# Kernel optimization log

Hardware: AMD Instinct MI355X
Metric: run time of the kernel (lower is better)

Reference implementation:

```python
import jax, jax.numpy as jnp
import numpy as np
import math

B, T, C = 4, 2048, 1024
NH = 16
HD = C // NH


def setup_inputs() -> dict:
    key = jax.random.key(0)
    ks = jax.random.split(key, 10)
    s = 0.02
    x = jax.random.normal(ks[0], (B, T, C), dtype=jnp.float32)
    W_qkv = jax.random.normal(ks[1], (C, 3 * C), dtype=jnp.float32) * s
    b_qkv = jnp.zeros((3 * C,), dtype=jnp.float32)
    W_proj = jax.random.normal(ks[2], (C, C), dtype=jnp.float32) * s
    b_proj = jnp.zeros((C,), dtype=jnp.float32)
    asym_mean, asym_std = 1.0, 0.7
    q_scale = jax.random.normal(ks[3], (NH, HD), dtype=jnp.float32) * asym_std + asym_mean
    q_bias = jax.random.normal(ks[4], (NH, HD), dtype=jnp.float32) * asym_std + asym_mean
    k_scale = jax.random.normal(ks[5], (NH, HD), dtype=jnp.float32) * asym_std + asym_mean
    k_bias = jax.random.normal(ks[6], (NH, HD), dtype=jnp.float32) * asym_std + asym_mean
    return {"x": x, "W_qkv": W_qkv, "b_qkv": b_qkv, "W_proj": W_proj,
            "b_proj": b_proj, "q_scale": q_scale, "q_bias": q_bias,
            "k_scale": k_scale, "k_bias": k_bias}


def reference(x, W_qkv, b_qkv, W_proj, b_proj, q_scale, q_bias, k_scale, k_bias):
    Bx, Tx, Cx = x.shape
    qkv = x @ W_qkv + b_qkv                       # [B,T,3C]
    q, k, v = jnp.split(qkv, 3, axis=-1)
    # [B,T,C] -> [B,NH,T,HD]
    reshape = lambda t: t.reshape(Bx, Tx, NH, HD).transpose(0, 2, 1, 3)
    q, k, v = reshape(q), reshape(k), reshape(v)
    # per-head affine scaling of Q/K
    q = q * q_scale[None, :, None, :] + q_bias[None, :, None, :]
    k = k * k_scale[None, :, None, :] + k_bias[None, :, None, :]
    scores = jnp.einsum('bhqd,bhkd->bhqk', q, k) / math.sqrt(HD)  # [B,NH,T,T]
    causal = jnp.tril(jnp.ones((Tx, Tx), dtype=bool))
    scores = jnp.where(causal[None, None], scores, -jnp.inf)
    att = jax.nn.softmax(scores, axis=-1)
    y = jnp.einsum('bhqk,bhkd->bhqd', att, v)     # [B,NH,T,HD]
    y = y.transpose(0, 2, 1, 3).reshape(Bx, Tx, Cx)
    return y @ W_proj + b_proj
```

## Files before the change

kernel.cpp:

```cpp
#include <hip/hip_runtime.h>
#include <hip/hip_bf16.h>

typedef unsigned short u16;
typedef __attribute__((ext_vector_type(8))) short short8;
typedef __attribute__((ext_vector_type(4))) float floatx4;

#define B_SZ 4
#define T_SZ 2048
#define C_SZ 1024
#define NH_SZ 16
#define HD_SZ 64
#define M_TOT 8192
#define K_DIM 1024

#define QSCALE 0.1803368801111204f

#define OFF_XB   ((size_t)16)
#define OFF_WQT  (OFF_XB + 8388608)
#define OFF_WPT  (OFF_WQT + 3145728)
#define OFF_PB   (OFF_WPT + 1048576)
#define OFF_Q    (OFF_PB + 8192)
#define OFF_K    (OFF_Q + 8388608)
#define OFF_V    (OFF_K + 8388608)
#define OFF_Y    (OFF_V + 8388608)
#define PB_BQKV  0
#define PB_BPROJ 3072
#define PB_QSC   4096
#define PB_QBI   5120
#define PB_KSC   6144
#define PB_KBI   7168

__device__ __forceinline__ float bf2f(u16 u) {
    return __uint_as_float(((unsigned)u) << 16);
}
__device__ __forceinline__ u16 f2bf(float f) {
    unsigned x = __float_as_uint(f);
    unsigned r = (x + 0x7fffu + ((x >> 16) & 1u)) >> 16;
    return (u16)r;
}
__device__ __forceinline__ u16 f2bf_fast(float f) {
    return (u16)((__float_as_uint(f) + 0x8000u) >> 16);
}
__device__ __forceinline__ void gl_lds16(const u16* g, u16* l) {
    __builtin_amdgcn_global_load_lds(
        (const __attribute__((address_space(1))) void*)g,
        (__attribute__((address_space(3))) void*)l, 16, 0, 0);
}

__global__ __launch_bounds__(256) void detect_k(const u16* __restrict__ x,
                                                int* __restrict__ flag) {
    __shared__ int cnt;
    if (threadIdx.x == 0) cnt = 0;
    __syncthreads();
    int bad = 0;
    for (int i = threadIdx.x; i < 512; i += 256) {
        float v = fabsf(bf2f(x[i]));
        if (v > 1024.0f || (v != 0.0f && v < 9.5367431640625e-7f)) bad++;
    }
    atomicAdd(&cnt, bad);
    __syncthreads();
    if (threadIdx.x == 0) flag[0] = (cnt > 16) ? 1 : 0;
}

__global__ __launch_bounds__(256) void prep_k(
        const void* __restrict__ x,
        const void* __restrict__ Wqkv, const void* __restrict__ Wproj,
        const void* __restrict__ bqkv, const void* __restrict__ bproj,
        const void* __restrict__ qsc, const void* __restrict__ qbi,
        const void* __restrict__ ksc, const void* __restrict__ kbi,
        u16* __restrict__ xb, u16* __restrict__ Wt_qkv,
        u16* __restrict__ Wt_proj, u16* __restrict__ pb,
        const int* __restrict__ flag) {
    __shared__ u16 t[32][33];
    const int blk = blockIdx.x;
    const int isf = flag[0];
    if (blk < 8192) {
        const int i = blk * 256 + threadIdx.x;
        if (isf) {
            const float4 v = ((const float4*)x)[i];
            ushort4 o;
            o.x = f2bf(v.x); o.y = f2bf(v.y); o.z = f2bf(v.z); o.w = f2bf(v.w);
            ((ushort4*)xb)[i] = o;
        } else {
            ((ushort4*)xb)[i] = ((const ushort4*)x)[i];
        }
        return;
    }
    if (blk < 8200) {
        const int i4 = (blk - 8192) * 256 + threadIdx.x;
        if (i4 >= 2048) return;
        const int e = i4 * 4;
        const void* src; int off;
        if (e < 3072)      { src = bqkv;  off = e; }
        else if (e < 4096) { src = bproj; off = e - 3072; }
        else if (e < 5120) { src = qsc;   off = e - 4096; }
        else if (e < 6144) { src = qbi;   off = e - 5120; }
        else if (e < 7168) { src = ksc;   off = e - 6144; }
        else               { src = kbi;   off = e - 7168; }
        ushort4 o;
        if (isf) {
            const float4 v = *(const float4*)((const float*)src + off);
            o.x = f2bf(v.x); o.y = f2bf(v.y); o.z = f2bf(v.z); o.w = f2bf(v.w);
        } else {
            o = *(const ushort4*)((const u16*)src + off);
        }
        *(ushort4*)&pb[e] = o;
        return;
    }
    const void* in; u16* out; int R, C, idx;
    if (blk < 11272) { idx = blk - 8200;  in = Wqkv;  out = Wt_qkv;  R = 1024; C = 3072; }
    else             { idx = blk - 11272; in = Wproj; out = Wt_proj; R = 1024; C = 1024; }
    const int nbx = C >> 5;
    const int c0 = (idx % nbx) * 32, r0 = (idx / nbx) * 32;
    const int tx = threadIdx.x & 31, ty = threadIdx.x >> 5;
    for (int i = 0; i < 4; i++) {
        int r = ty + i * 8;
        size_t gi = (size_t)(r0 + r) * C + c0 + tx;
        t[r][tx] = isf ? f2bf(((const float*)in)[gi]) : ((const u16*)in)[gi];
    }
    __syncthreads();
    for (int i = 0; i < 4; i++) {
        int cr = ty + i * 8;
        out[(size_t)(c0 + cr) * R + r0 + tx] = t[tx][cr];
    }
}

__global__ __launch_bounds__(256) void qkv_gemm(
        const u16* __restrict__ X, const u16* __restrict__ Wt,
        const u16* __restrict__ pb,
        u16* __restrict__ Qb, u16* __restrict__ Kb, u16* __restrict__ Vb) {
    __shared__ __align__(16) u16 As[128 * 64];
    __shared__ __align__(16) u16 Bs[128 * 64];
    const int bm = blockIdx.y * 128, bn = blockIdx.x * 128;
    const int tid = threadIdx.x;
    const int lane = tid & 63, wave = tid >> 6;
    const int quad = lane >> 4, l16 = lane & 15;
    const int wm = (wave & 1) * 64, wn = (wave >> 1) * 64;
    const int lrow = lane >> 3;
    const int lcol = ((lane & 7) ^ lrow) * 8;

    floatx4 acc[4][4];
    for (int mi = 0; mi < 4; mi++)
        for (int ni = 0; ni < 4; ni++) acc[mi][ni] = 0.f;

    for (int k0 = 0; k0 < K_DIM; k0 += 64) {
        __syncthreads();
        for (int j = 0; j < 4; j++) {
            const int rb = wave * 32 + j * 8;
            gl_lds16(&X[(size_t)(bm + rb + lrow) * K_DIM + k0 + lcol], &As[rb * 64]);
            gl_lds16(&Wt[(size_t)(bn + rb + lrow) * K_DIM + k0 + lcol], &Bs[rb * 64]);
        }
        __syncthreads();
        for (int kk = 0; kk < 64; kk += 32) {
            const int cb = kk >> 3;
            const int slot = ((cb + quad) ^ (l16 & 7)) * 8;
            short8 a[4], b[4];
            for (int mi = 0; mi < 4; mi++)
                a[mi] = *(const short8*)&As[(wm + mi * 16 + l16) * 64 + slot];
            for (int ni = 0; ni < 4; ni++)
                b[ni] = *(const short8*)&Bs[(wn + ni * 16 + l16) * 64 + slot];
            for (int mi = 0; mi < 4; mi++)
                for (int ni = 0; ni < 4; ni++)
                    acc[mi][ni] = __builtin_amdgcn_mfma_f32_16x16x32_bf16(
                        a[mi], b[ni], acc[mi][ni], 0, 0, 0);
        }
    }

    const int sec = bn >> 10;
    const int bb = bm >> 11;
    const int tbase = bm & 2047;
    for (int mi = 0; mi < 4; mi++) {
        for (int ni = 0; ni < 4; ni++) {
            const int col = bn + wn + ni * 16 + l16;
            const int cmod = col & 1023;
            const int h = cmod >> 6, d = cmod & 63;
            const float bv = bf2f(pb[PB_BQKV + col]);
            if (sec == 2) {
                const int t0 = tbase + wm + mi * 16 + quad * 4;
                ushort4 pk;
                pk.x = f2bf(acc[mi][ni][0] + bv);
                pk.y = f2bf(acc[mi][ni][1] + bv);
                pk.z = f2bf(acc[mi][ni][2] + bv);
                pk.w = f2bf(acc[mi][ni][3] + bv);
                *(ushort4*)&Vb[(((size_t)(bb * NH_SZ + h)) * HD_SZ + d) * T_SZ + t0] = pk;
            } else {
                float sA, sB;
                if (sec == 0) {
                    sA = bf2f(pb[PB_QSC + h * 64 + d]) * QSCALE;
                    sB = bf2f(pb[PB_QBI + h * 64 + d]) * QSCALE;
                } else {
                    sA = bf2f(pb[PB_KSC + h * 64 + d]);
                    sB = bf2f(pb[PB_KBI + h * 64 + d]);
                }
                u16* dstbuf = (sec == 0) ? Qb : Kb;
                for (int r = 0; r < 4; r++) {
                    const int t = tbase + wm + mi * 16 + quad * 4 + r;
                    float v = (acc[mi][ni][r] + bv) * sA + sB;
                    dstbuf[(((size_t)(bb * NH_SZ + h)) * T_SZ + t) * HD_SZ + d] = f2bf(v);
                }
            }
        }
    }
}

__global__ __launch_bounds__(512) void attn_k(const u16* __restrict__ Qb,
                                              const u16* __restrict__ Kb,
                                              const u16* __restrict__ Vtg,
                                              u16* __restrict__ Y) {
    __shared__ __align__(16) u16 Ks[64 * 64];
    __shared__ __align__(16) u16 Vs[64 * 64];
    __shared__ __align__(16) u16 Ps[8 * 16 * 88];
    const int blk = blockIdx.x;
    const int head = blk & 63;
    const int p = blk >> 6;
    const int b = head >> 4, h = head & 15;
    const int tid = threadIdx.x, lane = tid & 63, w = tid >> 6;
    const int quad = lane >> 4, l16 = lane & 15;
    const size_t qk_off = (size_t)head * (T_SZ * HD_SZ);
    const size_t v_off = (size_t)head * (HD_SZ * T_SZ);
    u16* psw = &Ps[w * 1408];
    const int lr = lane >> 3;
    const int lc = ((lane & 7) ^ lr) * 8;
    const int sl0 = ((quad) ^ (l16 & 7)) * 8;
    const int sl1 = ((4 + quad) ^ (l16 & 7)) * 8;

    short8 ones;
    for (int j = 0; j < 8; j++) ones[j] = (short)0x3F80;

    for (int tile = 0; tile < 2; tile++) {
        const int qt = tile ? p : (15 - p);
        const int q0 = qt * 128;
        const int rbase = q0 + w * 16;
        const int q = rbase + l16;

        const short8 aq0 = *(const short8*)&Qb[qk_off + (size_t)q * HD_SZ + quad * 8];
        const short8 aq1 = *(const short8*)&Qb[qk_off + (size_t)q * HD_SZ + 32 + quad * 8];

        floatx4 o[4];
        for (int mi = 0; mi < 4; mi++) o[mi] = 0.f;
        float m_run = -1e30f, l_run = 0.f;

        for (int k0 = 0; k0 < q0 + 128; k0 += 64) {
            __syncthreads();
            gl_lds16(&Kb[qk_off + (size_t)(k0 + w * 8 + lr) * HD_SZ + lc], &Ks[w * 512]);
            gl_lds16(&Vtg[v_off + (size_t)(w * 8 + lr) * T_SZ + k0 + lc], &Vs[w * 512]);
            __syncthreads();
            if (k0 > rbase + 15) continue;

            floatx4 s[4];
            for (int ni = 0; ni < 4; ni++) s[ni] = 0.f;
            for (int ni = 0; ni < 4; ni++)
                s[ni] = __builtin_amdgcn_mfma_f32_16x16x32_bf16(
                    *(const short8*)&Ks[(ni * 16 + l16) * 64 + sl0], aq0, s[ni], 0, 0, 0);
            for (int ni = 0; ni < 4; ni++)
                s[ni] = __builtin_amdgcn_mfma_f32_16x16x32_bf16(
                    *(const short8*)&Ks[(ni * 16 + l16) * 64 + sl1], aq1, s[ni], 0, 0, 0);

            if (k0 + 63 > rbase) {
                for (int ni = 0; ni < 4; ni++)
                    for (int r = 0; r < 4; r++) {
                        int key = k0 + ni * 16 + quad * 4 + r;
                        if (key > q) s[ni][r] = -1e30f;
                    }
            }

            float mx = fmaxf(fmaxf(s[0][0], s[0][1]), fmaxf(s[0][2], s[0][3]));
            for (int ni = 1; ni < 4; ni++)
                mx = fmaxf(mx, fmaxf(fmaxf(s[ni][0], s[ni][1]),
                                     fmaxf(s[ni][2], s[ni][3])));
            mx = fmaxf(mx, __shfl_xor(mx, 16, 64));
            mx = fmaxf(mx, __shfl_xor(mx, 32, 64));
            const float mnew = fmaxf(m_run, mx);
            const float alpha = exp2f(m_run - mnew);
            for (int ni = 0; ni < 4; ni++)
                for (int r = 0; r < 4; r++)
                    s[ni][r] = exp2f(s[ni][r] - mnew);
            m_run = mnew;
            for (int mi = 0; mi < 4; mi++) o[mi] *= alpha;

            for (int ni = 0; ni < 4; ni++) {
                ushort4 pk;
                pk.x = f2bf_fast(s[ni][0]); pk.y = f2bf_fast(s[ni][1]);
                pk.z = f2bf_fast(s[ni][2]); pk.w = f2bf_fast(s[ni][3]);
                *(ushort4*)&psw[l16 * 88 + ni * 16 + quad * 4] = pk;
            }

            floatx4 s4 = 0.f;
            for (int kk = 0; kk < 64; kk += 32) {
                short8 pfr = *(const short8*)&psw[l16 * 88 + kk + quad * 8];
                const int vsl = (kk == 0) ? sl0 : sl1;
                s4 = __builtin_amdgcn_mfma_f32_16x16x32_bf16(ones, pfr, s4, 0, 0, 0);
                for (int mi = 0; mi < 4; mi++) {
                    short8 vfr = *(const short8*)&Vs[(mi * 16 + l16) * 64 + vsl];
                    o[mi] = __builtin_amdgcn_mfma_f32_16x16x32_bf16(vfr, pfr, o[mi], 0, 0, 0);
                }
            }
            l_run = l_run * alpha + s4[0];
        }

        const float inv = 1.0f / l_run;
        u16* yrow = &Y[(((size_t)b * T_SZ + q) * NH_SZ + h) * HD_SZ];
        for (int mi = 0; mi < 4; mi++) {
            ushort4 pk;
            pk.x = f2bf_fast(o[mi][0] * inv); pk.y = f2bf_fast(o[mi][1] * inv);
            pk.z = f2bf_fast(o[mi][2] * inv); pk.w = f2bf_fast(o[mi][3] * inv);
            *(ushort4*)&yrow[mi * 16 + quad * 4] = pk;
        }
    }
}

__global__ __launch_bounds__(256) void proj_gemm(const u16* __restrict__ Yin,
                                                 const u16* __restrict__ Wt,
                                                 const u16* __restrict__ pb,
                                                 void* __restrict__ out,
                                                 const int* __restrict__ flag) {
    __shared__ __align__(16) u16 As[128 * 64];
    __shared__ __align__(16) u16 Bs[128 * 64];
    const int isf = flag[0];
    const int bm = blockIdx.y * 128, bn = blockIdx.x * 128;
    const int tid = threadIdx.x;
    const int lane = tid & 63, wave = tid >> 6;
    const int quad = lane >> 4, l16 = lane & 15;
    const int wm = (wave & 1) * 64, wn = (wave >> 1) * 64;
    const int lrow = lane >> 3;
    const int lcol = ((lane & 7) ^ lrow) * 8;

    floatx4 acc[4][4];
    for (int mi = 0; mi < 4; mi++)
        for (int ni = 0; ni < 4; ni++) acc[mi][ni] = 0.f;

    for (int k0 = 0; k0 < K_DIM; k0 += 64) {
        __syncthreads();
        for (int j = 0; j < 4; j++) {
            const int rb = wave * 32 + j * 8;
            gl_lds16(&Yin[(size_t)(bm + rb + lrow) * K_DIM + k0 + lcol], &As[rb * 64]);
            gl_lds16(&Wt[(size_t)(bn + rb + lrow) * K_DIM + k0 + lcol], &Bs[rb * 64]);
        }
        __syncthreads();
        for (int kk = 0; kk < 64; kk += 32) {
            const int cb = kk >> 3;
            const int slot = ((cb + quad) ^ (l16 & 7)) * 8;
            short8 a[4], b[4];
            for (int mi = 0; mi < 4; mi++)
                a[mi] = *(const short8*)&As[(wm + mi * 16 + l16) * 64 + slot];
            for (int ni = 0; ni < 4; ni++)
                b[ni] = *(const short8*)&Bs[(wn + ni * 16 + l16) * 64 + slot];
            for (int mi = 0; mi < 4; mi++)
                for (int ni = 0; ni < 4; ni++)
                    acc[mi][ni] = __builtin_amdgcn_mfma_f32_16x16x32_bf16(
                        a[mi], b[ni], acc[mi][ni], 0, 0, 0);
        }
    }

    for (int mi = 0; mi < 4; mi++) {
        for (int ni = 0; ni < 4; ni++) {
            const int col = bn + wn + ni * 16 + l16;
            const float bv = bf2f(pb[PB_BPROJ + col]);
            for (int r = 0; r < 4; r++) {
                const int row = bm + wm + mi * 16 + quad * 4 + r;
                const float v = acc[mi][ni][r] + bv;
                if (isf) ((float*)out)[(size_t)row * C_SZ + col] = v;
                else     ((u16*)out)[(size_t)row * C_SZ + col] = f2bf(v);
            }
        }
    }
}

extern "C" void kernel_launch(void* const* d_in, const int* in_sizes, int n_in,
                              void* d_out, int out_size, void* d_ws, size_t ws_size,
                              hipStream_t stream) {
    const void* x     = d_in[0];
    const void* Wqkv  = d_in[1];
    const void* bqkv  = d_in[2];
    const void* Wproj = d_in[3];
    const void* bproj = d_in[4];
    const void* qsc   = d_in[5];
    const void* qbi   = d_in[6];
    const void* ksc   = d_in[7];
    const void* kbi   = d_in[8];

    u16* ws = (u16*)d_ws;
    int* flag    = (int*)d_ws;
    u16* xb      = ws + OFF_XB;
    u16* Wt_qkv  = ws + OFF_WQT;
    u16* Wt_proj = ws + OFF_WPT;
    u16* pb      = ws + OFF_PB;
    u16* Qb      = ws + OFF_Q;
    u16* Kb      = ws + OFF_K;
    u16* Vb      = ws + OFF_V;
    u16* Yb      = ws + OFF_Y;

    detect_k<<<1, 256, 0, stream>>>((const u16*)x, flag);
    prep_k<<<12296, 256, 0, stream>>>(x, Wqkv, Wproj, bqkv, bproj,
                                      qsc, qbi, ksc, kbi,
                                      xb, Wt_qkv, Wt_proj, pb, flag);
    qkv_gemm<<<dim3(24, 64), 256, 0, stream>>>(xb, Wt_qkv, pb, Qb, Kb, Vb);
    attn_k<<<dim3(512), 512, 0, stream>>>(Qb, Kb, Vb, Yb);
    proj_gemm<<<dim3(8, 64), 256, 0, stream>>>(Yb, Wt_proj, pb, d_out, flag);
}
```

Measured before the change: 307.9 us.

## Double attention key tile to 128 with causal-aware active-key trimming; fold detect into prep

```diff
diff --git a/kernel.cpp b/kernel.cpp
--- a/kernel.cpp
+++ b/kernel.cpp
@@ -46,20 +46,13 @@
         (const __attribute__((address_space(1))) void*)g,
         (__attribute__((address_space(3))) void*)l, 16, 0, 0);
 }
-
-__global__ __launch_bounds__(256) void detect_k(const u16* __restrict__ x,
-                                                int* __restrict__ flag) {
-    __shared__ int cnt;
-    if (threadIdx.x == 0) cnt = 0;
-    __syncthreads();
-    int bad = 0;
-    for (int i = threadIdx.x; i < 512; i += 256) {
-        float v = fabsf(bf2f(x[i]));
-        if (v > 1024.0f || (v != 0.0f && v < 9.5367431640625e-7f)) bad++;
-    }
-    atomicAdd(&cnt, bad);
-    __syncthreads();
-    if (threadIdx.x == 0) flag[0] = (cnt > 16) ? 1 : 0;
+__device__ __forceinline__ int detect_isf(const u16* xx, int lane) {
+    float v0 = fabsf(bf2f(xx[lane * 2]));
+    float v1 = fabsf(bf2f(xx[lane * 2 + 1]));
+    int b0 = (v0 > 1024.0f) || (v0 != 0.0f && v0 < 9.5367431640625e-7f);
+    int b1 = (v1 > 1024.0f) || (v1 != 0.0f && v1 < 9.5367431640625e-7f);
+    unsigned long long ba = __ballot(b0), bb = __ballot(b1);
+    return (__popcll(ba) + __popcll(bb)) > 8;
 }
 
 __global__ __launch_bounds__(256) void prep_k(
@@ -70,10 +63,11 @@
         const void* __restrict__ ksc, const void* __restrict__ kbi,
         u16* __restrict__ xb, u16* __restrict__ Wt_qkv,
         u16* __restrict__ Wt_proj, u16* __restrict__ pb,
-        const int* __restrict__ flag) {
+        int* __restrict__ flag) {
     __shared__ u16 t[32][33];
     const int blk = blockIdx.x;
-    const int isf = flag[0];
+    const int isf = detect_isf((const u16*)x, threadIdx.x & 63);
+    if (blk == 0 && threadIdx.x == 0) flag[0] = isf;
     if (blk < 8192) {
         const int i = blk * 256 + threadIdx.x;
         if (isf) {
@@ -207,9 +201,9 @@
                                               const u16* __restrict__ Kb,
                                               const u16* __restrict__ Vtg,
                                               u16* __restrict__ Y) {
-    __shared__ __align__(16) u16 Ks[64 * 64];
-    __shared__ __align__(16) u16 Vs[64 * 64];
-    __shared__ __align__(16) u16 Ps[8 * 16 * 88];
+    __shared__ __align__(16) u16 Ks[128 * 64];
+    __shared__ __align__(16) u16 Vs[64 * 128];
+    __shared__ __align__(16) u16 Ps[8 * 16 * 136];
     const int blk = blockIdx.x;
     const int head = blk & 63;
     const int p = blk >> 6;
@@ -218,11 +212,14 @@
     const int quad = lane >> 4, l16 = lane & 15;
     const size_t qk_off = (size_t)head * (T_SZ * HD_SZ);
     const size_t v_off = (size_t)head * (HD_SZ * T_SZ);
-    u16* psw = &Ps[w * 1408];
+    u16* psw = &Ps[w * 2176];
     const int lr = lane >> 3;
-    const int lc = ((lane & 7) ^ lr) * 8;
-    const int sl0 = ((quad) ^ (l16 & 7)) * 8;
-    const int sl1 = ((4 + quad) ^ (l16 & 7)) * 8;
+    const int lck = ((lane & 7) ^ lr) * 8;
+    const int vrow_in = lane >> 4;
+    const int vch = lane & 15;
+    const int e3 = l16 & 7;
+    const int sl0 = ((0 + quad) ^ e3) * 8;
+    const int sl1 = ((4 + quad) ^ e3) * 8;
 
     short8 ones;
     for (int j = 0; j < 8; j++) ones[j] = (short)0x3F80;
@@ -240,58 +237,69 @@
         for (int mi = 0; mi < 4; mi++) o[mi] = 0.f;
         float m_run = -1e30f, l_run = 0.f;
 
-        for (int k0 = 0; k0 < q0 + 128; k0 += 64) {
+        for (int k0 = 0; k0 < q0 + 128; k0 += 128) {
             __syncthreads();
-            gl_lds16(&Kb[qk_off + (size_t)(k0 + w * 8 + lr) * HD_SZ + lc], &Ks[w * 512]);
-            gl_lds16(&Vtg[v_off + (size_t)(w * 8 + lr) * T_SZ + k0 + lc], &Vs[w * 512]);
+            for (int j = 0; j < 2; j++) {
+                gl_lds16(&Kb[qk_off + (size_t)(k0 + w * 16 + j * 8 + lr) * HD_SZ + lck],
+                         &Ks[(w * 16 + j * 8) * 64]);
+                const int dr = w * 8 + j * 4 + vrow_in;
+                gl_lds16(&Vtg[v_off + (size_t)dr * T_SZ + k0 + ((vch ^ (dr & 7)) * 8)],
+                         &Vs[(w * 8 + j * 4) * 128]);
+            }
             __syncthreads();
-            if (k0 > rbase + 15) continue;
-
-            floatx4 s[4];
-            for (int ni = 0; ni < 4; ni++) s[ni] = 0.f;
-            for (int ni = 0; ni < 4; ni++)
+            const int ak_raw = rbase + 16 - k0;
+            if (ak_raw <= 0) continue;
+            const int akeys = (ak_raw < 128) ? ak_raw : 128;
+            const int nact = akeys >> 4;
+            const bool diag = (ak_raw <= 128);
+
+            floatx4 s[8];
+            for (int ni = 0; ni < nact; ni++) s[ni] = 0.f;
+            for (int ni = 0; ni < nact; ni++)
                 s[ni] = __builtin_amdgcn_mfma_f32_16x16x32_bf16(
                     *(const short8*)&Ks[(ni * 16 + l16) * 64 + sl0], aq0, s[ni], 0, 0, 0);
-            for (int ni = 0; ni < 4; ni++)
+            for (int ni = 0; ni < nact; ni++)
                 s[ni] = __builtin_amdgcn_mfma_f32_16x16x32_bf16(
                     *(const short8*)&Ks[(ni * 16 + l16) * 64 + sl1], aq1, s[ni], 0, 0, 0);
 
-            if (k0 + 63 > rbase) {
-                for (int ni = 0; ni < 4; ni++)
-                    for (int r = 0; r < 4; r++) {
-                        int key = k0 + ni * 16 + quad * 4 + r;
-                        if (key > q) s[ni][r] = -1e30f;
-                    }
-            }
-
-            float mx = fmaxf(fmaxf(s[0][0], s[0][1]), fmaxf(s[0][2], s[0][3]));
-            for (int ni = 1; ni < 4; ni++)
+            if (diag) {
+                const int nd = nact - 1;
+                for (int r = 0; r < 4; r++)
+                    if (quad * 4 + r > l16) s[nd][r] = -1e30f;
+            }
+
+            float mx = -1e30f;
+            for (int ni = 0; ni < nact; ni++)
                 mx = fmaxf(mx, fmaxf(fmaxf(s[ni][0], s[ni][1]),
                                      fmaxf(s[ni][2], s[ni][3])));
             mx = fmaxf(mx, __shfl_xor(mx, 16, 64));
             mx = fmaxf(mx, __shfl_xor(mx, 32, 64));
             const float mnew = fmaxf(m_run, mx);
             const float alpha = exp2f(m_run - mnew);
-            for (int ni = 0; ni < 4; ni++)
+            for (int ni = 0; ni < nact; ni++)
                 for (int r = 0; r < 4; r++)
                     s[ni][r] = exp2f(s[ni][r] - mnew);
             m_run = mnew;
             for (int mi = 0; mi < 4; mi++) o[mi] *= alpha;
 
-            for (int ni = 0; ni < 4; ni++) {
+            for (int ni = 0; ni < 8; ni++) {
                 ushort4 pk;
-                pk.x = f2bf_fast(s[ni][0]); pk.y = f2bf_fast(s[ni][1]);
-                pk.z = f2bf_fast(s[ni][2]); pk.w = f2bf_fast(s[ni][3]);
-                *(ushort4*)&psw[l16 * 88 + ni * 16 + quad * 4] = pk;
+                if (ni < nact) {
+                    pk.x = f2bf_fast(s[ni][0]); pk.y = f2bf_fast(s[ni][1]);
+                    pk.z = f2bf_fast(s[ni][2]); pk.w = f2bf_fast(s[ni][3]);
+                } else {
+                    pk.x = 0; pk.y = 0; pk.z = 0; pk.w = 0;
+                }
+                *(ushort4*)&psw[l16 * 136 + ni * 16 + quad * 4] = pk;
             }
 
             floatx4 s4 = 0.f;
-            for (int kk = 0; kk < 64; kk += 32) {
-                short8 pfr = *(const short8*)&psw[l16 * 88 + kk + quad * 8];
-                const int vsl = (kk == 0) ? sl0 : sl1;
+            for (int kk = 0; kk < akeys; kk += 32) {
+                short8 pfr = *(const short8*)&psw[l16 * 136 + kk + quad * 8];
                 s4 = __builtin_amdgcn_mfma_f32_16x16x32_bf16(ones, pfr, s4, 0, 0, 0);
+                const int vsl = (((kk >> 3) + quad) ^ e3) * 8;
                 for (int mi = 0; mi < 4; mi++) {
-                    short8 vfr = *(const short8*)&Vs[(mi * 16 + l16) * 64 + vsl];
+                    short8 vfr = *(const short8*)&Vs[(mi * 16 + l16) * 128 + vsl];
                     o[mi] = __builtin_amdgcn_mfma_f32_16x16x32_bf16(vfr, pfr, o[mi], 0, 0, 0);
                 }
             }
@@ -390,7 +398,6 @@
     u16* Vb      = ws + OFF_V;
     u16* Yb      = ws + OFF_Y;
 
-    detect_k<<<1, 256, 0, stream>>>((const u16*)x, flag);
     prep_k<<<12296, 256, 0, stream>>>(x, Wqkv, Wproj, bqkv, bproj,
                                       qsc, qbi, ksc, kbi,
                                       xb, Wt_qkv, Wt_proj, pb, flag);
```

Result: slower. 464.5 us (+50.8%).
